# Kernel tuning notes

Measured on AMD Instinct MI355X. Metric: run time of the kernel, lower is better.

Reference implementation:

```python
import jax, jax.numpy as jnp
import numpy as np

BSZ, DIM, SEQ_A, SEQ_B = 16, 768, 1024, 1024


def setup_inputs() -> dict:
    key = jax.random.key(0)
    kA, kB, kU = jax.random.split(key, 3)
    input_A = jax.random.normal(kA, (BSZ, DIM, SEQ_A), dtype=jnp.float32)
    input_B = jax.random.normal(kB, (BSZ, DIM, SEQ_B), dtype=jnp.float32)
    intput_msk = jnp.zeros((BSZ, SEQ_A, SEQ_B), dtype=jnp.float32)  # 0 = on, -inf = off
    U = jax.random.normal(kU, (DIM, DIM), dtype=jnp.float32)
    return {"input_A": input_A, "input_B": input_B, "intput_msk": intput_msk, "U": U}


def reference(input_A, input_B, intput_msk, U):
    # align[b,s,t] = tanh( A[b,:,s]^T U B[b,:,t] )  -> (bsz, seq_A, seq_B)
    align = jnp.einsum("bds,de,bet->bst", input_A, U, input_B)
    align = jnp.tanh(align) + intput_msk
    # per-token scores: max over the other modality's sequence, then softmax
    score_A = jax.nn.softmax(jnp.max(align, axis=2), axis=-1)  # (bsz, seq_A)
    score_B = jax.nn.softmax(jnp.max(align, axis=1), axis=-1)  # (bsz, seq_B)
    output_A = jnp.einsum("bds,bs->bd", input_A, score_A)  # (bsz, dim_A)
    output_B = jnp.einsum("bdt,bt->bd", input_B, score_B)  # (bsz, dim_B)
    return (output_A, output_B)
```

## Files before the change

kernel.cpp:

```cpp
#include <hip/hip_runtime.h>
#include <math.h>

#define BSZ  16
#define DIM  768
#define SEQA 1024
#define SEQB 1024

typedef float f32x4 __attribute__((ext_vector_type(4)));
typedef long long llong;

__device__ inline void gload_lds16(const void* g, void* l) {
    __builtin_amdgcn_global_load_lds(
        (const __attribute__((address_space(1))) void*)g,
        (__attribute__((address_space(3))) void*)l, 16, 0, 0);
}

__device__ inline unsigned enc_key(float f) {
    unsigned u = __float_as_uint(f);
    return (u & 0x80000000u) ? ~u : (u | 0x80000000u);
}
__device__ inline float dec_key(unsigned k) {
    return (k & 0x80000000u) ? __uint_as_float(k ^ 0x80000000u) : __uint_as_float(~k);
}

__device__ inline unsigned pk4_fp8(float a, float b, float c, float d) {
    int v = 0;
    v = __builtin_amdgcn_cvt_pk_fp8_f32(a, b, v, false);
    v = __builtin_amdgcn_cvt_pk_fp8_f32(c, d, v, true);
    return (unsigned)v;
}
__device__ inline unsigned char f2fp8(float a) {
    return (unsigned char)(__builtin_amdgcn_cvt_pk_fp8_f32(a, a, 0, false) & 0xFF);
}

__device__ inline float fast_tanh(float x) {
    float ax = fabsf(x);
    float u = __expf(-2.0f * ax);
    float th = __fdividef(1.0f - u, 1.0f + u);
    return copysignf(th, x);
}

__global__ __launch_bounds__(256) void t_cast_AB(const float* __restrict__ A,
                                                 const float* __restrict__ B,
                                                 unsigned char* __restrict__ At,
                                                 unsigned char* __restrict__ Bt) {
    __shared__ float tl[64 * 65];
    const int z = blockIdx.z;
    const float* X = (z < BSZ) ? A : B;
    unsigned char* Y = (z < BSZ) ? At : Bt;
    const int b = z & 15;
    const int d0 = blockIdx.y * 64;
    const int s0 = blockIdx.x * 64;
    const int tid = threadIdx.x;
    const int rr = tid >> 4, c4 = tid & 15;
    const float* Xb = X + ((size_t)b * DIM + d0) * SEQA + s0;
#pragma unroll
    for (int i = 0; i < 4; i++) {
        int d = i * 16 + rr;
        float4 v = *(const float4*)&Xb[(size_t)d * SEQA + c4 * 4];
        tl[(c4 * 4 + 0) * 65 + d] = v.x;
        tl[(c4 * 4 + 1) * 65 + d] = v.y;
        tl[(c4 * 4 + 2) * 65 + d] = v.z;
        tl[(c4 * 4 + 3) * 65 + d] = v.w;
    }
    __syncthreads();
    unsigned char* Yb = Y + ((size_t)b * SEQA + s0) * DIM + d0;
    const int m = tid & 15, sl = tid >> 4;
#pragma unroll
    for (int i = 0; i < 4; i++) {
        int s = sl + 16 * i;
        unsigned v = pk4_fp8(tl[s * 65 + 4 * m + 0], tl[s * 65 + 4 * m + 1],
                             tl[s * 65 + 4 * m + 2], tl[s * 65 + 4 * m + 3]);
        *(unsigned*)&Yb[(size_t)s * DIM + 4 * m] = v;
    }
}

__global__ __launch_bounds__(256) void t_cast_U(const float* __restrict__ U,
                                                unsigned char* __restrict__ Ut,
                                                unsigned* __restrict__ keyA,
                                                unsigned* __restrict__ keyB) {
    __shared__ float tl[64][68];
    const int d0 = blockIdx.y * 64;
    const int e0 = blockIdx.x * 64;
    const int tid = threadIdx.x;
    const int bid = blockIdx.y * gridDim.x + blockIdx.x;
    if (bid < 64) {
        int i = bid * 256 + tid;
        keyA[i] = 0u;
        keyB[i] = 0u;
    }
    const int rr = tid >> 4, c4 = tid & 15;
#pragma unroll
    for (int i = 0; i < 4; i++) {
        int row = i * 16 + rr;
        float4 v = *(const float4*)&U[(size_t)(d0 + row) * DIM + e0 + c4 * 4];
        *(float4*)&tl[row][c4 * 4] = v;
    }
    __syncthreads();
    const int m = tid & 15, sl = tid >> 4;
#pragma unroll
    for (int i = 0; i < 4; i++) {
        int e = sl + 16 * i;
        unsigned v = pk4_fp8(tl[4 * m + 0][e], tl[4 * m + 1][e], tl[4 * m + 2][e], tl[4 * m + 3][e]);
        *(unsigned*)&Ut[(size_t)(e0 + e) * DIM + d0 + 4 * m] = v;
    }
}

__device__ inline void stage_tile(const unsigned char* __restrict__ src, int row0,
                                  int kbyte0, unsigned char* lds, int wid, int lane) {
    const int r8 = lane >> 3;
    const int g  = lane & 7;
    const int gg = g ^ (r8 & 7);
#pragma unroll
    for (int t = 0; t < 4; ++t) {
        int row = row0 + wid * 32 + t * 8 + r8;
        gload_lds16(src + (size_t)row * DIM + kbyte0 + gg * 16,
                    lds + (wid * 32 + t * 8) * 128 + lane * 16);
    }
}

__device__ inline llong frag_read(const unsigned char* lds, int rowbase, int l15,
                                  int quad, int h) {
    int gg = 2 * h + (quad >> 1);
    int off = (rowbase + l15) * 128 + ((gg ^ (l15 & 7)) << 4) + (quad & 1) * 8;
    return *(const llong*)(lds + off);
}

__global__ __launch_bounds__(256, 3) void k1_ua(const unsigned char* __restrict__ At,
                                                const unsigned char* __restrict__ Ut,
                                                unsigned char* __restrict__ Ct) {
    __shared__ __align__(16) unsigned char As[128 * 128];
    __shared__ __align__(16) unsigned char Us[128 * 128];
    const int b  = blockIdx.z;
    const int s0 = blockIdx.x * 128;
    const int e0 = blockIdx.y * 128;
    const int tid = threadIdx.x;
    const int lane = tid & 63;
    const int wid = tid >> 6;
    const int wr = wid >> 1, wc = wid & 1;
    const int quad = lane >> 4, l15 = lane & 15;

    const unsigned char* Atb = At + (size_t)b * SEQA * DIM;
    f32x4 acc[4][4] = {};

    for (int d0 = 0; d0 < DIM; d0 += 128) {
        stage_tile(Atb + (size_t)s0 * DIM, 0, d0, As, wid, lane);
        stage_tile(Ut + (size_t)e0 * DIM, 0, d0, Us, wid, lane);
        __syncthreads();
#pragma unroll
        for (int h = 0; h < 4; ++h) {
            llong av[4], bv[4];
#pragma unroll
            for (int i = 0; i < 4; ++i) av[i] = frag_read(As, wr * 64 + 16 * i, l15, quad, h);
#pragma unroll
            for (int j = 0; j < 4; ++j) bv[j] = frag_read(Us, wc * 64 + 16 * j, l15, quad, h);
#pragma unroll
            for (int i = 0; i < 4; ++i)
#pragma unroll
                for (int j = 0; j < 4; ++j)
                    acc[i][j] = __builtin_amdgcn_mfma_f32_16x16x32_fp8_fp8(av[i], bv[j], acc[i][j], 0, 0, 0);
        }
        __syncthreads();
    }
    unsigned char* Cb = Ct + (size_t)b * SEQA * DIM;
#pragma unroll
    for (int i = 0; i < 4; ++i)
#pragma unroll
        for (int j = 0; j < 4; ++j) {
            int e_g = e0 + wc * 64 + 16 * j + l15;
#pragma unroll
            for (int r = 0; r < 4; ++r) {
                int s_g = s0 + wr * 64 + 16 * i + quad * 4 + r;
                Cb[(size_t)s_g * DIM + e_g] = f2fp8(acc[i][j][r]);
            }
        }
}

__global__ __launch_bounds__(256, 4) void k2_align(const unsigned char* __restrict__ Ct,
                                                   const unsigned char* __restrict__ Bt,
                                                   const float* __restrict__ msk,
                                                   unsigned* __restrict__ keyA,
                                                   unsigned* __restrict__ keyB) {
    __shared__ __align__(16) unsigned char Cs[128 * 128];
    __shared__ __align__(16) unsigned char Bs[128 * 128];
    const int b  = blockIdx.z;
    const int t0 = blockIdx.x * 128;
    const int s0 = blockIdx.y * 128;
    const int tid = threadIdx.x;
    const int lane = tid & 63;
    const int wid = tid >> 6;
    const int wr = wid >> 1, wc = wid & 1;
    const int quad = lane >> 4, l15 = lane & 15;

    f32x4 acc[4][4] = {};

    for (int e0 = 0; e0 < DIM; e0 += 128) {
        stage_tile(Ct + (size_t)(b * SEQA + s0) * DIM, 0, e0, Cs, wid, lane);
        stage_tile(Bt + (size_t)(b * SEQB + t0) * DIM, 0, e0, Bs, wid, lane);
        __syncthreads();
#pragma unroll
        for (int h = 0; h < 4; ++h) {
            llong av[4], bv[4];
#pragma unroll
            for (int i = 0; i < 4; ++i) av[i] = frag_read(Bs, wr * 64 + 16 * i, l15, quad, h);
#pragma unroll
            for (int j = 0; j < 4; ++j) bv[j] = frag_read(Cs, wc * 64 + 16 * j, l15, quad, h);
#pragma unroll
            for (int i = 0; i < 4; ++i)
#pragma unroll
                for (int j = 0; j < 4; ++j)
                    acc[i][j] = __builtin_amdgcn_mfma_f32_16x16x32_fp8_fp8(av[i], bv[j], acc[i][j], 0, 0, 0);
        }
        __syncthreads();
    }

    const float* Mb = msk + (size_t)b * SEQA * SEQB;
#pragma unroll
    for (int j = 0; j < 4; ++j) {
        int s_g = s0 + wc * 64 + 16 * j + l15;
#pragma unroll
        for (int i = 0; i < 4; ++i) {
            int t_g = t0 + wr * 64 + 16 * i + quad * 4;
            float4 mvv = *(const float4*)&Mb[(size_t)s_g * SEQB + t_g];
            acc[i][j][0] += mvv.x;
            acc[i][j][1] += mvv.y;
            acc[i][j][2] += mvv.z;
            acc[i][j][3] += mvv.w;
        }
    }
#pragma unroll
    for (int j = 0; j < 4; ++j) {
        float m = -INFINITY;
#pragma unroll
        for (int i = 0; i < 4; ++i)
#pragma unroll
            for (int r = 0; r < 4; ++r) m = fmaxf(m, acc[i][j][r]);
        m = fmaxf(m, __shfl_xor(m, 16));
        m = fmaxf(m, __shfl_xor(m, 32));
        if (quad == 0) {
            float kv = (m == -INFINITY) ? m : fast_tanh(m);
            atomicMax(&keyA[b * SEQA + s0 + wc * 64 + 16 * j + l15], enc_key(kv));
        }
    }
#pragma unroll
    for (int i = 0; i < 4; ++i)
#pragma unroll
        for (int r = 0; r < 4; ++r) {
            float m = fmaxf(fmaxf(acc[i][0][r], acc[i][1][r]), fmaxf(acc[i][2][r], acc[i][3][r]));
            m = fmaxf(m, __shfl_xor(m, 1));
            m = fmaxf(m, __shfl_xor(m, 2));
            m = fmaxf(m, __shfl_xor(m, 4));
            m = fmaxf(m, __shfl_xor(m, 8));
            if (l15 == 0) {
                float kv = (m == -INFINITY) ? m : fast_tanh(m);
                atomicMax(&keyB[b * SEQB + t0 + wr * 64 + 16 * i + quad * 4 + r], enc_key(kv));
            }
        }
}

__global__ __launch_bounds__(256) void k3_softmax(const unsigned* __restrict__ keyA,
                                                  const unsigned* __restrict__ keyB,
                                                  float* __restrict__ scoreA,
                                                  float* __restrict__ scoreB) {
    const int b = blockIdx.x;
    const bool isA = (blockIdx.y == 0);
    const unsigned* keys = isA ? (keyA + b * SEQA) : (keyB + b * SEQB);
    float* score = isA ? (scoreA + b * SEQA) : (scoreB + b * SEQB);
    __shared__ float sh[4];
    const int tid = threadIdx.x;
    float m[4];
    float mx = -INFINITY;
#pragma unroll
    for (int k = 0; k < 4; k++) {
        m[k] = dec_key(keys[tid + 256 * k]);
        mx = fmaxf(mx, m[k]);
    }
#pragma unroll
    for (int o = 32; o > 0; o >>= 1) mx = fmaxf(mx, __shfl_down(mx, o, 64));
    if ((tid & 63) == 0) sh[tid >> 6] = mx;
    __syncthreads();
    mx = fmaxf(fmaxf(sh[0], sh[1]), fmaxf(sh[2], sh[3]));
    __syncthreads();
    float e[4];
    float sum = 0.f;
#pragma unroll
    for (int k = 0; k < 4; k++) { e[k] = expf(m[k] - mx); sum += e[k]; }
#pragma unroll
    for (int o = 32; o > 0; o >>= 1) sum += __shfl_down(sum, o, 64);
    if ((tid & 63) == 0) sh[tid >> 6] = sum;
    __syncthreads();
    sum = sh[0] + sh[1] + sh[2] + sh[3];
    float inv = 1.0f / sum;
#pragma unroll
    for (int k = 0; k < 4; k++) score[tid + 256 * k] = e[k] * inv;
}

__global__ __launch_bounds__(256) void k4_out(const float* __restrict__ A,
                                              const float* __restrict__ B,
                                              const float* __restrict__ scoreA,
                                              const float* __restrict__ scoreB,
                                              float* __restrict__ out) {
    const int which = blockIdx.y;
    const int row = blockIdx.x * 4 + (threadIdx.x >> 6);
    const int lane = threadIdx.x & 63;
    const float* X = which ? B : A;
    const float* S = which ? scoreB : scoreA;
    const int b = row / DIM;
    const float4* xr = (const float4*)(X + (size_t)row * SEQA);
    const float4* sr = (const float4*)(S + (size_t)b * SEQA);
    float acc = 0.f;
#pragma unroll
    for (int q = lane; q < SEQA / 4; q += 64) {
        float4 x = xr[q];
        float4 s = sr[q];
        acc += x.x * s.x + x.y * s.y + x.z * s.z + x.w * s.w;
    }
#pragma unroll
    for (int o = 32; o > 0; o >>= 1) acc += __shfl_down(acc, o, 64);
    if (lane == 0) out[which * (BSZ * DIM) + row] = acc;
}

extern "C" void kernel_launch(void* const* d_in, const int* in_sizes, int n_in,
                              void* d_out, int out_size, void* d_ws, size_t ws_size,
                              hipStream_t stream) {
    const float* A   = (const float*)d_in[0];
    const float* B   = (const float*)d_in[1];
    const float* msk = (const float*)d_in[2];
    const float* U   = (const float*)d_in[3];
    float* out = (float*)d_out;

    char* ws = (char*)d_ws;
    unsigned char* At = (unsigned char*)ws;
    unsigned char* Bt = (unsigned char*)(ws + 12582912);
    unsigned char* Ct = (unsigned char*)(ws + 25165824);
    unsigned char* Ut = (unsigned char*)(ws + 37748736);
    unsigned* keyA   = (unsigned*)(ws + 38338560);
    unsigned* keyB   = (unsigned*)(ws + 38404096);
    float*    scoreA = (float*)   (ws + 38469632);
    float*    scoreB = (float*)   (ws + 38535168);

    t_cast_U<<<dim3(DIM / 64, DIM / 64, 1), 256, 0, stream>>>(U, Ut, keyA, keyB);
    t_cast_AB<<<dim3(SEQA / 64, DIM / 64, 2 * BSZ), 256, 0, stream>>>(A, B, At, Bt);
    k1_ua<<<dim3(SEQA / 128, DIM / 128, BSZ), 256, 0, stream>>>(At, Ut, Ct);
    k2_align<<<dim3(SEQB / 128, SEQA / 128, BSZ), 256, 0, stream>>>(Ct, Bt, msk, keyA, keyB);
    k3_softmax<<<dim3(BSZ, 2), 256, 0, stream>>>(keyA, keyB, scoreA, scoreB);
    k4_out<<<dim3(BSZ * DIM / 4, 2), 256, 0, stream>>>(A, B, scoreA, scoreB, out);
}
```

Baseline: 238.9 us.

## Merge cast kernels, overlap B cast with UA GEMM, fuse softmax into output

The U cast and key zeroing are folded into the A cast kernel. The B transpose-cast blocks are interleaved with the A·U GEMM blocks in one launch, one GEMM block per five. The softmax is recomputed per block inside the output-reduction kernel, and the scores go to shared memory instead of global. This cuts the launch count from six to four and lets memory-bound cast work overlap compute-bound MFMA work, at the cost of redundant softmax work in every output block.

```diff
diff --git a/kernel.cpp b/kernel.cpp
--- a/kernel.cpp
+++ b/kernel.cpp
@@ -40,69 +40,66 @@
     return copysignf(th, x);
 }
 
-__global__ __launch_bounds__(256) void t_cast_AB(const float* __restrict__ A,
-                                                 const float* __restrict__ B,
-                                                 unsigned char* __restrict__ At,
-                                                 unsigned char* __restrict__ Bt) {
-    __shared__ float tl[64 * 65];
+__global__ __launch_bounds__(256) void cast_AU(const float* __restrict__ A,
+                                               const float* __restrict__ U,
+                                               unsigned char* __restrict__ At,
+                                               unsigned char* __restrict__ Ut,
+                                               unsigned* __restrict__ keyA,
+                                               unsigned* __restrict__ keyB) {
+    __shared__ float tl[64 * 68];
     const int z = blockIdx.z;
-    const float* X = (z < BSZ) ? A : B;
-    unsigned char* Y = (z < BSZ) ? At : Bt;
-    const int b = z & 15;
-    const int d0 = blockIdx.y * 64;
-    const int s0 = blockIdx.x * 64;
     const int tid = threadIdx.x;
-    const int rr = tid >> 4, c4 = tid & 15;
-    const float* Xb = X + ((size_t)b * DIM + d0) * SEQA + s0;
-#pragma unroll
-    for (int i = 0; i < 4; i++) {
-        int d = i * 16 + rr;
-        float4 v = *(const float4*)&Xb[(size_t)d * SEQA + c4 * 4];
-        tl[(c4 * 4 + 0) * 65 + d] = v.x;
-        tl[(c4 * 4 + 1) * 65 + d] = v.y;
-        tl[(c4 * 4 + 2) * 65 + d] = v.z;
-        tl[(c4 * 4 + 3) * 65 + d] = v.w;
-    }
-    __syncthreads();
-    unsigned char* Yb = Y + ((size_t)b * SEQA + s0) * DIM + d0;
-    const int m = tid & 15, sl = tid >> 4;
-#pragma unroll
-    for (int i = 0; i < 4; i++) {
-        int s = sl + 16 * i;
-        unsigned v = pk4_fp8(tl[s * 65 + 4 * m + 0], tl[s * 65 + 4 * m + 1],
-                             tl[s * 65 + 4 * m + 2], tl[s * 65 + 4 * m + 3]);
-        *(unsigned*)&Yb[(size_t)s * DIM + 4 * m] = v;
-    }
-}
-
-__global__ __launch_bounds__(256) void t_cast_U(const float* __restrict__ U,
-                                                unsigned char* __restrict__ Ut,
-                                                unsigned* __restrict__ keyA,
-                                                unsigned* __restrict__ keyB) {
-    __shared__ float tl[64][68];
-    const int d0 = blockIdx.y * 64;
-    const int e0 = blockIdx.x * 64;
-    const int tid = threadIdx.x;
-    const int bid = blockIdx.y * gridDim.x + blockIdx.x;
-    if (bid < 64) {
-        int i = bid * 256 + tid;
-        keyA[i] = 0u;
-        keyB[i] = 0u;
-    }
-    const int rr = tid >> 4, c4 = tid & 15;
-#pragma unroll
-    for (int i = 0; i < 4; i++) {
-        int row = i * 16 + rr;
-        float4 v = *(const float4*)&U[(size_t)(d0 + row) * DIM + e0 + c4 * 4];
-        *(float4*)&tl[row][c4 * 4] = v;
-    }
-    __syncthreads();
-    const int m = tid & 15, sl = tid >> 4;
-#pragma unroll
-    for (int i = 0; i < 4; i++) {
-        int e = sl + 16 * i;
-        unsigned v = pk4_fp8(tl[4 * m + 0][e], tl[4 * m + 1][e], tl[4 * m + 2][e], tl[4 * m + 3][e]);
-        *(unsigned*)&Ut[(size_t)(e0 + e) * DIM + d0 + 4 * m] = v;
+    if (z < BSZ) {
+        const int b = z;
+        const int d0 = blockIdx.y * 64;
+        const int s0 = blockIdx.x * 64;
+        const int rr = tid >> 4, c4 = tid & 15;
+        const float* Xb = A + ((size_t)b * DIM + d0) * SEQA + s0;
+#pragma unroll
+        for (int i = 0; i < 4; i++) {
+            int d = i * 16 + rr;
+            float4 v = *(const float4*)&Xb[(size_t)d * SEQA + c4 * 4];
+            tl[(c4 * 4 + 0) * 65 + d] = v.x;
+            tl[(c4 * 4 + 1) * 65 + d] = v.y;
+            tl[(c4 * 4 + 2) * 65 + d] = v.z;
+            tl[(c4 * 4 + 3) * 65 + d] = v.w;
+        }
+        __syncthreads();
+        unsigned char* Yb = At + ((size_t)b * SEQA + s0) * DIM + d0;
+        const int m = tid & 15, sl = tid >> 4;
+#pragma unroll
+        for (int i = 0; i < 4; i++) {
+            int s = sl + 16 * i;
+            unsigned v = pk4_fp8(tl[s * 65 + 4 * m + 0], tl[s * 65 + 4 * m + 1],
+                                 tl[s * 65 + 4 * m + 2], tl[s * 65 + 4 * m + 3]);
+            *(unsigned*)&Yb[(size_t)s * DIM + 4 * m] = v;
+        }
+    } else {
+        if (blockIdx.x >= 12) return;
+        const int d0 = blockIdx.y * 64;
+        const int e0 = blockIdx.x * 64;
+        const int bid = blockIdx.y * 12 + blockIdx.x;
+        if (bid < 64) {
+            int i = bid * 256 + tid;
+            keyA[i] = 0u;
+            keyB[i] = 0u;
+        }
+        const int rr = tid >> 4, c4 = tid & 15;
+#pragma unroll
+        for (int i = 0; i < 4; i++) {
+            int row = i * 16 + rr;
+            float4 v = *(const float4*)&U[(size_t)(d0 + row) * DIM + e0 + c4 * 4];
+            *(float4*)&tl[row * 68 + c4 * 4] = v;
+        }
+        __syncthreads();
+        const int m = tid & 15, sl = tid >> 4;
+#pragma unroll
+        for (int i = 0; i < 4; i++) {
+            int e = sl + 16 * i;
+            unsigned v = pk4_fp8(tl[(4 * m + 0) * 68 + e], tl[(4 * m + 1) * 68 + e],
+                                 tl[(4 * m + 2) * 68 + e], tl[(4 * m + 3) * 68 + e]);
+            *(unsigned*)&Ut[(size_t)(e0 + e) * DIM + d0 + 4 * m] = v;
+        }
     }
 }
 
@@ -126,54 +123,88 @@
     return *(const llong*)(lds + off);
 }
 
-__global__ __launch_bounds__(256, 3) void k1_ua(const unsigned char* __restrict__ At,
-                                                const unsigned char* __restrict__ Ut,
-                                                unsigned char* __restrict__ Ct) {
-    __shared__ __align__(16) unsigned char As[128 * 128];
-    __shared__ __align__(16) unsigned char Us[128 * 128];
-    const int b  = blockIdx.z;
-    const int s0 = blockIdx.x * 128;
-    const int e0 = blockIdx.y * 128;
+__global__ __launch_bounds__(256, 3) void k1_castB(const unsigned char* __restrict__ At,
+                                                   const unsigned char* __restrict__ Ut,
+                                                   unsigned char* __restrict__ Ct,
+                                                   const float* __restrict__ B,
+                                                   unsigned char* __restrict__ Bt) {
+    __shared__ __align__(16) unsigned char smem[32768];
+    const int gbid = blockIdx.x;
     const int tid = threadIdx.x;
-    const int lane = tid & 63;
-    const int wid = tid >> 6;
-    const int wr = wid >> 1, wc = wid & 1;
-    const int quad = lane >> 4, l15 = lane & 15;
-
-    const unsigned char* Atb = At + (size_t)b * SEQA * DIM;
-    f32x4 acc[4][4] = {};
-
-    for (int d0 = 0; d0 < DIM; d0 += 128) {
-        stage_tile(Atb + (size_t)s0 * DIM, 0, d0, As, wid, lane);
-        stage_tile(Ut + (size_t)e0 * DIM, 0, d0, Us, wid, lane);
-        __syncthreads();
-#pragma unroll
-        for (int h = 0; h < 4; ++h) {
-            llong av[4], bv[4];
-#pragma unroll
-            for (int i = 0; i < 4; ++i) av[i] = frag_read(As, wr * 64 + 16 * i, l15, quad, h);
-#pragma unroll
-            for (int j = 0; j < 4; ++j) bv[j] = frag_read(Us, wc * 64 + 16 * j, l15, quad, h);
-#pragma unroll
-            for (int i = 0; i < 4; ++i)
-#pragma unroll
-                for (int j = 0; j < 4; ++j)
-                    acc[i][j] = __builtin_amdgcn_mfma_f32_16x16x32_fp8_fp8(av[i], bv[j], acc[i][j], 0, 0, 0);
-        }
-        __syncthreads();
-    }
-    unsigned char* Cb = Ct + (size_t)b * SEQA * DIM;
-#pragma unroll
-    for (int i = 0; i < 4; ++i)
-#pragma unroll
-        for (int j = 0; j < 4; ++j) {
-            int e_g = e0 + wc * 64 + 16 * j + l15;
-#pragma unroll
-            for (int r = 0; r < 4; ++r) {
-                int s_g = s0 + wr * 64 + 16 * i + quad * 4 + r;
-                Cb[(size_t)s_g * DIM + e_g] = f2fp8(acc[i][j][r]);
+    if (gbid % 5 == 0) {
+        const int kid = gbid / 5;
+        const int s0 = (kid & 7) * 128;
+        const int e0 = ((kid >> 3) % 6) * 128;
+        const int b  = kid / 48;
+        unsigned char* As = smem;
+        unsigned char* Us = smem + 16384;
+        const int lane = tid & 63;
+        const int wid = tid >> 6;
+        const int wr = wid >> 1, wc = wid & 1;
+        const int quad = lane >> 4, l15 = lane & 15;
+
+        const unsigned char* Atb = At + (size_t)b * SEQA * DIM;
+        f32x4 acc[4][4] = {};
+
+        for (int d0 = 0; d0 < DIM; d0 += 128) {
+            stage_tile(Atb + (size_t)s0 * DIM, 0, d0, As, wid, lane);
+            stage_tile(Ut + (size_t)e0 * DIM, 0, d0, Us, wid, lane);
+            __syncthreads();
+#pragma unroll
+            for (int h = 0; h < 4; ++h) {
+                llong av[4], bv[4];
+#pragma unroll
+                for (int i = 0; i < 4; ++i) av[i] = frag_read(As, wr * 64 + 16 * i, l15, quad, h);
+#pragma unroll
+                for (int j = 0; j < 4; ++j) bv[j] = frag_read(Us, wc * 64 + 16 * j, l15, quad, h);
+#pragma unroll
+                for (int i = 0; i < 4; ++i)
+#pragma unroll
+                    for (int j = 0; j < 4; ++j)
+                        acc[i][j] = __builtin_amdgcn_mfma_f32_16x16x32_fp8_fp8(av[i], bv[j], acc[i][j], 0, 0, 0);
             }
-        }
+            __syncthreads();
+        }
+        unsigned char* Cb = Ct + (size_t)b * SEQA * DIM;
+#pragma unroll
+        for (int i = 0; i < 4; ++i)
+#pragma unroll
+            for (int j = 0; j < 4; ++j) {
+                int e_g = e0 + wc * 64 + 16 * j + l15;
+#pragma unroll
+                for (int r = 0; r < 4; ++r) {
+                    int s_g = s0 + wr * 64 + 16 * i + quad * 4 + r;
+                    Cb[(size_t)s_g * DIM + e_g] = f2fp8(acc[i][j][r]);
+                }
+            }
+    } else {
+        const int cid = gbid - gbid / 5 - 1;
+        const int s0 = (cid & 15) * 64;
+        const int d0 = ((cid >> 4) % 12) * 64;
+        const int b  = cid / 192;
+        float* tl = (float*)smem;
+        const int rr = tid >> 4, c4 = tid & 15;
+        const float* Xb = B + ((size_t)b * DIM + d0) * SEQA + s0;
+#pragma unroll
+        for (int i = 0; i < 4; i++) {
+            int d = i * 16 + rr;
+            float4 v = *(const float4*)&Xb[(size_t)d * SEQA + c4 * 4];
+            tl[(c4 * 4 + 0) * 65 + d] = v.x;
+            tl[(c4 * 4 + 1) * 65 + d] = v.y;
+            tl[(c4 * 4 + 2) * 65 + d] = v.z;
+            tl[(c4 * 4 + 3) * 65 + d] = v.w;
+        }
+        __syncthreads();
+        unsigned char* Yb = Bt + ((size_t)b * SEQA + s0) * DIM + d0;
+        const int m = tid & 15, sl = tid >> 4;
+#pragma unroll
+        for (int i = 0; i < 4; i++) {
+            int s = sl + 16 * i;
+            unsigned v = pk4_fp8(tl[s * 65 + 4 * m + 0], tl[s * 65 + 4 * m + 1],
+                                 tl[s * 65 + 4 * m + 2], tl[s * 65 + 4 * m + 3]);
+            *(unsigned*)&Yb[(size_t)s * DIM + 4 * m] = v;
+        }
+    }
 }
 
 __global__ __launch_bounds__(256, 4) void k2_align(const unsigned char* __restrict__ Ct,
@@ -258,16 +289,20 @@
         }
 }
 
-__global__ __launch_bounds__(256) void k3_softmax(const unsigned* __restrict__ keyA,
-                                                  const unsigned* __restrict__ keyB,
-                                                  float* __restrict__ scoreA,
-                                                  float* __restrict__ scoreB) {
-    const int b = blockIdx.x;
-    const bool isA = (blockIdx.y == 0);
-    const unsigned* keys = isA ? (keyA + b * SEQA) : (keyB + b * SEQB);
-    float* score = isA ? (scoreA + b * SEQA) : (scoreB + b * SEQB);
-    __shared__ float sh[4];
+__global__ __launch_bounds__(256) void k4s(const float* __restrict__ A,
+                                           const float* __restrict__ B,
+                                           const unsigned* __restrict__ keyA,
+                                           const unsigned* __restrict__ keyB,
+                                           float* __restrict__ out) {
+    __shared__ __align__(16) float sc[1024];
+    __shared__ float red[4];
+    const int which = blockIdx.y;
     const int tid = threadIdx.x;
+    const int lane = tid & 63;
+    const int row = blockIdx.x * 4 + (tid >> 6);
+    const int b = (blockIdx.x * 4) / DIM;
+
+    const unsigned* keys = which ? (keyB + b * SEQB) : (keyA + b * SEQA);
     float m[4];
     float mx = -INFINITY;
 #pragma unroll
@@ -277,42 +312,31 @@
     }
 #pragma unroll
     for (int o = 32; o > 0; o >>= 1) mx = fmaxf(mx, __shfl_down(mx, o, 64));
-    if ((tid & 63) == 0) sh[tid >> 6] = mx;
+    if (lane == 0) red[tid >> 6] = mx;
     __syncthreads();
-    mx = fmaxf(fmaxf(sh[0], sh[1]), fmaxf(sh[2], sh[3]));
+    mx = fmaxf(fmaxf(red[0], red[1]), fmaxf(red[2], red[3]));
     __syncthreads();
-    float e[4];
+    float e4[4];
     float sum = 0.f;
 #pragma unroll
-    for (int k = 0; k < 4; k++) { e[k] = expf(m[k] - mx); sum += e[k]; }
+    for (int k = 0; k < 4; k++) { e4[k] = expf(m[k] - mx); sum += e4[k]; }
 #pragma unroll
     for (int o = 32; o > 0; o >>= 1) sum += __shfl_down(sum, o, 64);
-    if ((tid & 63) == 0) sh[tid >> 6] = sum;
+    if (lane == 0) red[tid >> 6] = sum;
     __syncthreads();
-    sum = sh[0] + sh[1] + sh[2] + sh[3];
+    sum = red[0] + red[1] + red[2] + red[3];
     float inv = 1.0f / sum;
 #pragma unroll
-    for (int k = 0; k < 4; k++) score[tid + 256 * k] = e[k] * inv;
-}
-
-__global__ __launch_bounds__(256) void k4_out(const float* __restrict__ A,
-                                              const float* __restrict__ B,
-                                              const float* __restrict__ scoreA,
-                                              const float* __restrict__ scoreB,
-                                              float* __restrict__ out) {
-    const int which = blockIdx.y;
-    const int row = blockIdx.x * 4 + (threadIdx.x >> 6);
-    const int lane = threadIdx.x & 63;
+    for (int k = 0; k < 4; k++) sc[tid + 256 * k] = e4[k] * inv;
+    __syncthreads();
+
     const float* X = which ? B : A;
-    const float* S = which ? scoreB : scoreA;
-    const int b = row / DIM;
     const float4* xr = (const float4*)(X + (size_t)row * SEQA);
-    const float4* sr = (const float4*)(S + (size_t)b * SEQA);
     float acc = 0.f;
 #pragma unroll
     for (int q = lane; q < SEQA / 4; q += 64) {
         float4 x = xr[q];
-        float4 s = sr[q];
+        float4 s = *(const float4*)&sc[q * 4];
         acc += x.x * s.x + x.y * s.y + x.z * s.z + x.w * s.w;
     }
 #pragma unroll
@@ -336,13 +360,9 @@
     unsigned char* Ut = (unsigned char*)(ws + 37748736);
     unsigned* keyA   = (unsigned*)(ws + 38338560);
     unsigned* keyB   = (unsigned*)(ws + 38404096);
-    float*    scoreA = (float*)   (ws + 38469632);
-    float*    scoreB = (float*)   (ws + 38535168);
-
-    t_cast_U<<<dim3(DIM / 64, DIM / 64, 1), 256, 0, stream>>>(U, Ut, keyA, keyB);
-    t_cast_AB<<<dim3(SEQA / 64, DIM / 64, 2 * BSZ), 256, 0, stream>>>(A, B, At, Bt);
-    k1_ua<<<dim3(SEQA / 128, DIM / 128, BSZ), 256, 0, stream>>>(At, Ut, Ct);
+
+    cast_AU<<<dim3(SEQA / 64, DIM / 64, BSZ + 1), 256, 0, stream>>>(A, U, At, Ut, keyA, keyB);
+    k1_castB<<<dim3(3840, 1, 1), 256, 0, stream>>>(At, Ut, Ct, B, Bt);
     k2_align<<<dim3(SEQB / 128, SEQA / 128, BSZ), 256, 0, stream>>>(Ct, Bt, msk, keyA, keyB);
-    k3_softmax<<<dim3(BSZ, 2), 256, 0, stream>>>(keyA, keyB, scoreA, scoreB);
-    k4_out<<<dim3(BSZ * DIM / 4, 2), 256, 0, stream>>>(A, B, scoreA, scoreB, out);
-}
+    k4s<<<dim3(BSZ * DIM / 4, 2), 256, 0, stream>>>(A, B, keyA, keyB, out);
+}
```

After: 231.6 us. -3.1%, faster.
